# Optimization experiments

Measured on AMD Instinct MI355X. Metric: run time of the kernel, lower is better.

Reference implementation:

```python
import jax, jax.numpy as jnp
import numpy as np

WS = 3
HEADS = 6
C = 192
QK_UNITS = 32
QKC = HEADS * QK_UNITS      # 192
V_UNITS = C // HEADS        # 32
DIL = 1
EPS = 1.55e-05


def _static_kernel():
    # one-hot im2col kernel: output tap i picks window offset (i//WS, i%WS)
    sk = np.zeros((WS, WS, 1, WS * WS), np.float32)
    for i in range(WS * WS):
        sk[i // WS, i % WS, 0, i] = 1.0
    return jnp.asarray(sk)


def _depthwise(x, kernel, dil):
    # TF depthwise_conv2d: kernel [ws,ws,Cin,mult] -> out channel c*mult+m
    ws, _, cin, mult = kernel.shape
    k = kernel.reshape(ws, ws, 1, cin * mult)
    return jax.lax.conv_general_dilated(
        x, k, window_strides=(1, 1), padding='SAME',
        rhs_dilation=(dil, dil),
        dimension_numbers=('NHWC', 'HWIO', 'NHWC'),
        feature_group_count=cin)


def _rel_bias(cpb_w1, cpb_b1, cpb_w2):
    # RelativeBias(query_window=1, key_window=WS, pretrain_window=WS)
    halo = (WS - 1) // 2
    rel = np.arange(-halo, halo + 1, dtype=np.float32)
    rel = np.stack(np.meshgrid(rel, rel, indexing='ij'), axis=-1)  # [WS,WS,2]
    rel = rel * (8.0 / (WS - 1.0))
    rel = np.sign(rel) * np.log1p(np.abs(rel)) / np.log(8.0)
    tab = jnp.asarray(rel.reshape(-1, 2))                 # [WS^2, 2]
    hid = jax.nn.relu(tab @ cpb_w1 + cpb_b1)              # CPB MLP
    bias = jax.nn.sigmoid(hid @ cpb_w2) * 16.0            # [WS^2, HEADS]
    # for query_window==1 the rel_idx gather is a row reversal of the table
    bias = bias[::-1]
    return bias.T                                         # [HEADS, WS^2]


def reference(x, qkv_w, q_bias, v_bias, deformable_kernel, scale,
              cpb_w1, cpb_b1, cpb_w2, proj_w, proj_b):
    B, H, W, _ = x.shape
    sk = _static_kernel()

    # 1x1 qkv conv + (q, 0, v) bias
    qkv = jnp.einsum('bhwc,cd->bhwd', x, qkv_w)
    qkv = qkv + jnp.concatenate([q_bias, jnp.zeros_like(q_bias), v_bias])
    q, k, v = jnp.split(qkv, [QKC, 2 * QKC], axis=-1)

    # deformable + static window extraction (depthwise, multiplier = WS^2)
    k = _depthwise(k, deformable_kernel + sk, DIL)        # [B,H,W,QKC*WS^2]
    v_kernel = deformable_kernel
    if C != QKC:
        v_kernel = jnp.repeat(v_kernel, C // QKC, axis=2)
    v = _depthwise(v, sk + v_kernel, DIL)                 # [B,H,W,C*WS^2]

    q = q.reshape(B, H, W, HEADS, 1, QK_UNITS)
    k = k.reshape(B, H, W, HEADS, QK_UNITS, WS * WS)
    v = v.reshape(B, H, W, HEADS, V_UNITS, WS * WS)

    # tf.math.l2_normalize semantics: x * rsqrt(max(sum(x^2), eps))
    q = q * jax.lax.rsqrt(jnp.maximum(jnp.sum(q * q, -1, keepdims=True), EPS))
    k = k * jax.lax.rsqrt(jnp.maximum(jnp.sum(k * k, -2, keepdims=True), EPS))

    attn = jnp.matmul(q * jnp.exp(scale), k)              # [B,H,W,HEADS,1,WS^2]

    # border mask: zero-padded taps get -100
    ones = jnp.ones((1, H, W, 1), x.dtype)
    valid = _depthwise(ones, sk, DIL).reshape(1, H, W, 1, 1, WS * WS)
    mask = -100.0 * (valid == 0.0).astype(x.dtype)
    rb = _rel_bias(cpb_w1, cpb_b1, cpb_w2).reshape(1, 1, 1, HEADS, 1, WS * WS)
    attn = jax.nn.softmax(attn + mask + rb, axis=-1)

    out = jnp.matmul(attn, jnp.swapaxes(v, -1, -2))       # [B,H,W,HEADS,1,V_UNITS]
    out = out.reshape(B, H, W, C)
    return jnp.einsum('bhwc,cd->bhwd', out, proj_w) + proj_b


def setup_inputs() -> dict:
    key = jax.random.key(0)
    ks = jax.random.split(key, 6)
    return {
        'x': jax.random.normal(ks[0], (4, 96, 96, C), jnp.float32),
        'qkv_w': jax.random.normal(ks[1], (C, 2 * QKC + C), jnp.float32) * (C ** -0.5),
        'q_bias': jnp.zeros((QKC,), jnp.float32),
        'v_bias': jnp.zeros((C,), jnp.float32),
        'deformable_kernel': jax.random.normal(ks[2], (WS, WS, QKC, WS * WS), jnp.float32) * 0.05,
        'scale': jnp.full((HEADS, 1, 1), np.log(10.0), jnp.float32),
        'cpb_w1': jax.random.normal(ks[3], (2, 512), jnp.float32) * 0.5,
        'cpb_b1': jnp.zeros((512,), jnp.float32),
        'cpb_w2': jax.random.normal(ks[4], (512, HEADS), jnp.float32) * (512 ** -0.5),
        'proj_w': jax.random.normal(ks[5], (C, C), jnp.float32) * (C ** -0.5),
        'proj_b': jnp.zeros((C,), jnp.float32),
    }
```

## Files before the change

kernel.cpp:

```cpp
#include <hip/hip_runtime.h>
#include <math.h>

#define EPS 1.55e-05f
#define PIX 36864
#define IMG 9216

typedef __attribute__((ext_vector_type(8))) short short8v;
typedef __attribute__((ext_vector_type(4))) float float4v;
typedef __attribute__((ext_vector_type(4))) unsigned short ushort4v;
typedef __attribute__((ext_vector_type(4))) unsigned int uint4v;

static __device__ __forceinline__ unsigned short f2bf(float f) {
    unsigned u = __float_as_uint(f);
    unsigned r = (u + 0x7FFFu + ((u >> 16) & 1u)) >> 16;
    return (unsigned short)r;
}
static __device__ __forceinline__ float bflo(unsigned d) {
    return __uint_as_float(d << 16);
}
static __device__ __forceinline__ float bfhi(unsigned d) {
    return __uint_as_float(d & 0xffff0000u);
}

__global__ __launch_bounds__(512)
void relbias_kernel(const float* __restrict__ w1, const float* __restrict__ b1,
                    const float* __restrict__ w2, float* __restrict__ rb)
{
    __shared__ float hid[9][512];
    int i = threadIdx.x;
    const float s0 = -0.7739760316291208f, s2 = 0.7739760316291208f;
    float sv[3]; sv[0] = s0; sv[1] = 0.f; sv[2] = s2;
    float w1a = w1[i], w1b = w1[512 + i], bb = b1[i];
    #pragma unroll
    for (int j = 0; j < 9; j++) {
        float t0 = sv[j / 3], t1 = sv[j % 3];
        hid[j][i] = fmaxf(t0 * w1a + t1 * w1b + bb, 0.f);
    }
    __syncthreads();
    if (i < 54) {
        int he = i / 9, t = i % 9, j = 8 - t;
        float acc = 0.f;
        for (int u = 0; u < 512; u++) acc += hid[j][u] * w2[u * 6 + he];
        rb[he * 9 + t] = 16.f / (1.f + expf(-acc));
    }
}

__global__ __launch_bounds__(256)
void prep_kernel(const float* __restrict__ x, const float* __restrict__ qkv_w,
                 const float* __restrict__ proj_w,
                 unsigned short* __restrict__ xs, unsigned short* __restrict__ Bt,
                 unsigned short* __restrict__ Bt2)
{
    int tid = blockIdx.x * 256 + threadIdx.x;
    int stride = gridDim.x * 256;
    int total_x4 = PIX * 192 / 4;
    for (int i = tid; i < total_x4; i += stride) {
        float4 v = ((const float4*)x)[i];
        ushort4v o;
        o.x = f2bf(v.x); o.y = f2bf(v.y); o.z = f2bf(v.z); o.w = f2bf(v.w);
        ((ushort4v*)xs)[i] = o;
    }
    for (int i = tid; i < 576 * 192; i += stride) {
        int n = i / 192, k = i - n * 192;
        Bt[i] = f2bf(qkv_w[k * 576 + n]);
    }
    for (int i = tid; i < 192 * 192; i += stride) {
        int n = i / 192, k = i - n * 192;
        Bt2[i] = f2bf(proj_w[k * 192 + n]);
    }
}

template<int MODE>
__global__ __launch_bounds__(256)
void mfma_gemm_kernel(const unsigned short* __restrict__ Abf,
                      const unsigned short* __restrict__ Btb,
                      void* __restrict__ Cout,
                      const float* __restrict__ bias0,
                      const float* __restrict__ bias1)
{
    const int K = 192;
    __shared__ short smem[128 * 64 + 64 * 64];
    short* As = smem;
    short* Bs = smem + 128 * 64;
    int tid = threadIdx.x;
    int m0 = blockIdx.y * 128;
    int n0 = blockIdx.x * 64;
    int lane = tid & 63, wid = tid >> 6;
    int wm = wid >> 1, wn = wid & 1;
    int lr = lane & 15, lk = lane >> 4;

    float4v acc[4][2];
    #pragma unroll
    for (int a = 0; a < 4; a++)
        #pragma unroll
        for (int b = 0; b < 2; b++)
            #pragma unroll
            for (int e = 0; e < 4; e++) acc[a][b][e] = 0.f;

    int sr = tid >> 3;
    int sc = tid & 7;
    for (int k0 = 0; k0 < K; k0 += 64) {
        #pragma unroll
        for (int i = 0; i < 4; i++) {
            int r = sr + i * 32;
            short8v v = *(const short8v*)(Abf + (size_t)(m0 + r) * K + k0 + sc * 8);
            *(short8v*)(As + r * 64 + ((sc ^ (r & 7)) * 8)) = v;
        }
        #pragma unroll
        for (int i = 0; i < 2; i++) {
            int r = sr + i * 32;
            short8v v = *(const short8v*)(Btb + (size_t)(n0 + r) * K + k0 + sc * 8);
            *(short8v*)(Bs + r * 64 + ((sc ^ (r & 7)) * 8)) = v;
        }
        __syncthreads();
        #pragma unroll
        for (int ks = 0; ks < 2; ks++) {
            short8v af[4], bf[2];
            #pragma unroll
            for (int fm = 0; fm < 4; fm++) {
                int r = wm * 64 + fm * 16 + lr;
                int c = (ks * 4 + lk) ^ (r & 7);
                af[fm] = *(const short8v*)(As + r * 64 + c * 8);
            }
            #pragma unroll
            for (int fn = 0; fn < 2; fn++) {
                int r = wn * 32 + fn * 16 + lr;
                int c = (ks * 4 + lk) ^ (r & 7);
                bf[fn] = *(const short8v*)(Bs + r * 64 + c * 8);
            }
            #pragma unroll
            for (int fm = 0; fm < 4; fm++)
                #pragma unroll
                for (int fn = 0; fn < 2; fn++)
                    acc[fm][fn] = __builtin_amdgcn_mfma_f32_16x16x32_bf16(
                        af[fm], bf[fn], acc[fm][fn], 0, 0, 0);
        }
        __syncthreads();
    }

    if (MODE == 0) {
        const int TP = 74;
        unsigned short* T = (unsigned short*)smem;
        #pragma unroll
        for (int fm = 0; fm < 4; fm++) {
            #pragma unroll
            for (int fn = 0; fn < 2; fn++) {
                int n = wn * 32 + fn * 16 + lr;
                int gn = n0 + n;
                float bv = (gn < 192) ? bias0[gn] : ((gn < 384) ? 0.f : bias1[gn - 384]);
                #pragma unroll
                for (int e = 0; e < 4; e++) {
                    int m = wm * 64 + fm * 16 + lk * 4 + e;
                    T[m * TP + n] = f2bf(acc[fm][fn][e] + bv);
                }
            }
        }
        __syncthreads();
        unsigned short* qkv8 = (unsigned short*)Cout;
        #pragma unroll
        for (int i = 0; i < 4; i++) {
            int u = tid + 256 * i;
            int m = u & 127, cgl = u >> 7;
            short8v vv = *(const short8v*)(T + m * TP + cgl * 8);
            int gcg = (n0 >> 3) + cgl;
            *(short8v*)(qkv8 + ((size_t)gcg * PIX + m0 + m) * 8) = vv;
        }
    } else {
        float* outp = (float*)Cout;
        #pragma unroll
        for (int fm = 0; fm < 4; fm++) {
            #pragma unroll
            for (int fn = 0; fn < 2; fn++) {
                int n = n0 + wn * 32 + fn * 16 + lr;
                float bv = bias0[n];
                #pragma unroll
                for (int e = 0; e < 4; e++) {
                    int m = m0 + wm * 64 + fm * 16 + lk * 4 + e;
                    outp[(size_t)m * 192 + n] = acc[fm][fn][e] + bv;
                }
            }
        }
    }
}

__global__ __launch_bounds__(256)
void fused5_kernel(const unsigned short* __restrict__ qkv8, const float* __restrict__ deform,
                   const float* __restrict__ scale, const float* __restrict__ rb,
                   unsigned short* __restrict__ attnS)
{
    __shared__ float red[64][21];

    int id = blockIdx.x;
    int strip = id % 3;
    int yp = (id / 3) % 48;
    int he = (id / 144) % 6;
    int b = id / 864;
    int tid = threadIdx.x;
    int l = tid & 63;
    int wsub = tid >> 6;
    int X = strip * 32 + (l & 31);
    int Y = yp * 2 + (l >> 5);
    int pimg = Y * 96 + X;
    size_t ibase = (size_t)b * IMG;

    for (int i = tid; i < 64 * 21; i += 256) (&red[0][0])[i] = 0.f;
    __syncthreads();

    int c0 = __builtin_amdgcn_readfirstlane(he * 32 + wsub * 8);
    int qg = c0 >> 3;
    const uint4v* qp = (const uint4v*)(qkv8 + ((size_t)qg * PIX + ibase) * 8);
    const uint4v* kp = (const uint4v*)(qkv8 + ((size_t)(24 + qg) * PIX + ibase) * 8);
    const uint4v* vp = (const uint4v*)(qkv8 + ((size_t)(48 + qg) * PIX + ibase) * 8);

    int off[9];
    unsigned okm = 0;
    #pragma unroll
    for (int pos = 0; pos < 9; pos++) {
        int dy = pos / 3 - 1, dx = pos % 3 - 1;
        int yy = Y + dy, xx = X + dx;
        bool ok = (yy >= 0) && (yy < 96) && (xx >= 0) && (xx < 96);
        okm |= (ok ? 1u : 0u) << pos;
        off[pos] = ok ? (yy * 96 + xx) : pimg;
    }

    uint4v qd = qp[pimg];
    uint4v kd[9];
    #pragma unroll
    for (int pos = 0; pos < 9; pos++) kd[pos] = kp[off[pos]];
    #pragma unroll
    for (int pos = 0; pos < 9; pos++)
        if (!((okm >> pos) & 1)) { kd[pos].x = 0; kd[pos].y = 0; kd[pos].z = 0; kd[pos].w = 0; }

    float qk[9], kn[9];
    #pragma unroll
    for (int t = 0; t < 9; t++) { qk[t] = 0.f; kn[t] = 0.f; }
    float qn2 = 0.f;

    #pragma unroll
    for (int ci = 0; ci < 8; ci++) {
        int c = c0 + ci;
        unsigned qw = ((const unsigned*)&qd)[ci >> 1];
        float q = (ci & 1) ? bfhi(qw) : bflo(qw);
        qn2 = fmaf(q, q, qn2);
        float kin[9];
        #pragma unroll
        for (int pos = 0; pos < 9; pos++) {
            unsigned dw = ((const unsigned*)&kd[pos])[ci >> 1];
            kin[pos] = (ci & 1) ? bfhi(dw) : bflo(dw);
        }
        float ktap[9];
        #pragma unroll
        for (int t = 0; t < 9; t++) ktap[t] = kin[t];
        #pragma unroll
        for (int pos = 0; pos < 9; pos++) {
            const float* wr = deform + ((size_t)pos * 192 + c) * 9;
            #pragma unroll
            for (int t = 0; t < 9; t++) ktap[t] = fmaf(kin[pos], wr[t], ktap[t]);
        }
        #pragma unroll
        for (int t = 0; t < 9; t++) {
            qk[t] = fmaf(q, ktap[t], qk[t]);
            kn[t] = fmaf(ktap[t], ktap[t], kn[t]);
        }
    }

    uint4v vd[9];
    #pragma unroll
    for (int pos = 0; pos < 9; pos++) vd[pos] = vp[off[pos]];

    #pragma unroll
    for (int t = 0; t < 9; t++) atomicAdd(&red[l][t], qk[t]);
    #pragma unroll
    for (int t = 0; t < 9; t++) atomicAdd(&red[l][9 + t], kn[t]);
    atomicAdd(&red[l][18], qn2);

    #pragma unroll
    for (int pos = 0; pos < 9; pos++)
        if (!((okm >> pos) & 1)) { vd[pos].x = 0; vd[pos].y = 0; vd[pos].z = 0; vd[pos].w = 0; }
    __syncthreads();

    float qn = rsqrtf(fmaxf(red[l][18], EPS));
    float es = expf(scale[he]);
    float w[9];
    float m = -1e30f;
    #pragma unroll
    for (int t = 0; t < 9; t++) {
        float lg = es * qn * red[l][t] * rsqrtf(fmaxf(red[l][9 + t], EPS));
        lg += (((okm >> t) & 1) ? 0.f : -100.f) + rb[he * 9 + t];
        w[t] = lg;
        m = fmaxf(m, lg);
    }
    float ssum = 0.f;
    #pragma unroll
    for (int t = 0; t < 9; t++) { w[t] = expf(w[t] - m); ssum += w[t]; }
    float inv = 1.f / ssum;
    #pragma unroll
    for (int t = 0; t < 9; t++) w[t] *= inv;

    unsigned short o8[8];
    #pragma unroll
    for (int ci = 0; ci < 8; ci++) {
        int c = c0 + ci;
        float vin[9];
        #pragma unroll
        for (int pos = 0; pos < 9; pos++) {
            unsigned dw = ((const unsigned*)&vd[pos])[ci >> 1];
            vin[pos] = (ci & 1) ? bfhi(dw) : bflo(dw);
        }
        float acc = 0.f;
        #pragma unroll
        for (int pos = 0; pos < 9; pos++) {
            const float* wr = deform + ((size_t)pos * 192 + c) * 9;
            float sp = w[pos];
            #pragma unroll
            for (int t = 0; t < 9; t++) sp = fmaf(w[t], wr[t], sp);
            acc = fmaf(vin[pos], sp, acc);
        }
        o8[ci] = f2bf(acc);
    }
    short8v ov;
    #pragma unroll
    for (int ci = 0; ci < 8; ci++) ov[ci] = (short)o8[ci];
    *(short8v*)(attnS + (ibase + pimg) * 192 + c0) = ov;
}

extern "C" void kernel_launch(void* const* d_in, const int* in_sizes, int n_in,
                              void* d_out, int out_size, void* d_ws, size_t ws_size,
                              hipStream_t stream) {
    const float* x       = (const float*)d_in[0];
    const float* qkv_w   = (const float*)d_in[1];
    const float* q_bias  = (const float*)d_in[2];
    const float* v_bias  = (const float*)d_in[3];
    const float* deform  = (const float*)d_in[4];
    const float* scale   = (const float*)d_in[5];
    const float* cpb_w1  = (const float*)d_in[6];
    const float* cpb_b1  = (const float*)d_in[7];
    const float* cpb_w2  = (const float*)d_in[8];
    const float* proj_w  = (const float*)d_in[9];
    const float* proj_b  = (const float*)d_in[10];
    float* out = (float*)d_out;

    char* ws = (char*)d_ws;
    float*          rb    = (float*)ws;
    unsigned short* xs    = (unsigned short*)(ws + 256);
    unsigned short* Bt    = (unsigned short*)(ws + 256 + 14155776);
    unsigned short* Bt2   = (unsigned short*)(ws + 256 + 14155776 + 221184);
    unsigned short* qkv8  = (unsigned short*)(ws + 256 + 14155776 + 221184 + 73728);
    unsigned short* attnS = (unsigned short*)(ws + 256 + 14155776 + 221184 + 73728 + 42467328);

    relbias_kernel<<<1, 512, 0, stream>>>(cpb_w1, cpb_b1, cpb_w2, rb);
    prep_kernel<<<2048, 256, 0, stream>>>(x, qkv_w, proj_w, xs, Bt, Bt2);
    mfma_gemm_kernel<0><<<dim3(576 / 64, PIX / 128), 256, 0, stream>>>(
        xs, Bt, (void*)qkv8, q_bias, v_bias);
    fused5_kernel<<<3456, 256, 0, stream>>>(qkv8, deform, scale, rb, attnS);
    mfma_gemm_kernel<1><<<dim3(192 / 64, PIX / 128), 256, 0, stream>>>(
        attnS, Bt2, (void*)out, proj_b, nullptr);
}
```

Before: 291.9 us.

## Stage K/V halo tiles in LDS and use 2D pixel tiles per head

Replaces the fused window-attention kernel with a version that assigns each block a 16x4 pixel tile for one head. The block cooperatively loads the K and V halo (18x6 pixels times 32 channels) into shared memory, and neighbour taps are read from LDS instead of nine redundant global gathers per pixel. Each warp now handles 16 channels instead of 8, and blocks shrink to 128 threads. The aim is to cut redundant global and L2 traffic for overlapping 3x3 windows, at the cost of extra syncs, LDS use and more per-thread work.

After: 270.0 us. 7.5% less time.

```diff
diff --git a/kernel.cpp b/kernel.cpp
--- a/kernel.cpp
+++ b/kernel.cpp
@@ -15,12 +15,8 @@
     unsigned r = (u + 0x7FFFu + ((u >> 16) & 1u)) >> 16;
     return (unsigned short)r;
 }
-static __device__ __forceinline__ float bflo(unsigned d) {
-    return __uint_as_float(d << 16);
-}
-static __device__ __forceinline__ float bfhi(unsigned d) {
-    return __uint_as_float(d & 0xffff0000u);
-}
+static __device__ __forceinline__ float bflo(unsigned d) { return __uint_as_float(d << 16); }
+static __device__ __forceinline__ float bfhi(unsigned d) { return __uint_as_float(d & 0xffff0000u); }
 
 __global__ __launch_bounds__(512)
 void relbias_kernel(const float* __restrict__ w1, const float* __restrict__ b1,
@@ -183,53 +179,74 @@
     }
 }
 
-__global__ __launch_bounds__(256)
-void fused5_kernel(const unsigned short* __restrict__ qkv8, const float* __restrict__ deform,
+__global__ __launch_bounds__(128)
+void fused7_kernel(const unsigned short* __restrict__ qkv8, const float* __restrict__ deform,
                    const float* __restrict__ scale, const float* __restrict__ rb,
                    unsigned short* __restrict__ attnS)
 {
+    __shared__ unsigned short kv[4][108][8];
     __shared__ float red[64][21];
 
     int id = blockIdx.x;
-    int strip = id % 3;
-    int yp = (id / 3) % 48;
-    int he = (id / 144) % 6;
-    int b = id / 864;
+    int he = id % 6;
+    int tile = id / 6;
+    int b = tile / 144;
+    int t2 = tile - b * 144;
+    int x0 = (t2 % 6) * 16, y0 = (t2 / 6) * 4;
     int tid = threadIdx.x;
     int l = tid & 63;
-    int wsub = tid >> 6;
-    int X = strip * 32 + (l & 31);
-    int Y = yp * 2 + (l >> 5);
+    int w = __builtin_amdgcn_readfirstlane(tid >> 6);
+    int lx = l & 15, ly = l >> 4;
+    int X = x0 + lx, Y = y0 + ly;
     int pimg = Y * 96 + X;
     size_t ibase = (size_t)b * IMG;
 
-    for (int i = tid; i < 64 * 21; i += 256) (&red[0][0])[i] = 0.f;
+    for (int i = tid; i < 64 * 21; i += 128) (&red[0][0])[i] = 0.f;
+
+    int g8q = he * 4 + w * 2;
+    uint4v qd[2];
+    qd[0] = *(const uint4v*)(qkv8 + ((size_t)g8q * PIX + ibase + pimg) * 8);
+    qd[1] = *(const uint4v*)(qkv8 + ((size_t)(g8q + 1) * PIX + ibase + pimg) * 8);
+
+    int kgbase = 24 + he * 4;
+    int vgbase = 48 + he * 4;
+    #pragma unroll
+    for (int r = 0; r < 4; r++) {
+        int i = tid + r * 128;
+        if (i < 432) {
+            int gg = i / 108, hp = i - gg * 108;
+            int hy = hp / 18, hx = hp - hy * 18;
+            int gx = x0 - 1 + hx, gy = y0 - 1 + hy;
+            bool ok = (gx >= 0) && (gx < 96) && (gy >= 0) && (gy < 96);
+            uint4v v; v.x = 0; v.y = 0; v.z = 0; v.w = 0;
+            if (ok) v = *(const uint4v*)(qkv8 + ((size_t)(kgbase + gg) * PIX + ibase + gy * 96 + gx) * 8);
+            *(uint4v*)&kv[gg][hp][0] = v;
+        }
+    }
+    uint4v vst[4];
+    #pragma unroll
+    for (int r = 0; r < 4; r++) {
+        int i = tid + r * 128;
+        vst[r].x = 0; vst[r].y = 0; vst[r].z = 0; vst[r].w = 0;
+        if (i < 432) {
+            int gg = i / 108, hp = i - gg * 108;
+            int hy = hp / 18, hx = hp - hy * 18;
+            int gx = x0 - 1 + hx, gy = y0 - 1 + hy;
+            bool ok = (gx >= 0) && (gx < 96) && (gy >= 0) && (gy < 96);
+            if (ok) vst[r] = *(const uint4v*)(qkv8 + ((size_t)(vgbase + gg) * PIX + ibase + gy * 96 + gx) * 8);
+        }
+    }
     __syncthreads();
 
-    int c0 = __builtin_amdgcn_readfirstlane(he * 32 + wsub * 8);
-    int qg = c0 >> 3;
-    const uint4v* qp = (const uint4v*)(qkv8 + ((size_t)qg * PIX + ibase) * 8);
-    const uint4v* kp = (const uint4v*)(qkv8 + ((size_t)(24 + qg) * PIX + ibase) * 8);
-    const uint4v* vp = (const uint4v*)(qkv8 + ((size_t)(48 + qg) * PIX + ibase) * 8);
-
-    int off[9];
     unsigned okm = 0;
     #pragma unroll
     for (int pos = 0; pos < 9; pos++) {
         int dy = pos / 3 - 1, dx = pos % 3 - 1;
-        int yy = Y + dy, xx = X + dx;
-        bool ok = (yy >= 0) && (yy < 96) && (xx >= 0) && (xx < 96);
+        bool ok = (Y + dy >= 0) && (Y + dy < 96) && (X + dx >= 0) && (X + dx < 96);
         okm |= (ok ? 1u : 0u) << pos;
-        off[pos] = ok ? (yy * 96 + xx) : pimg;
-    }
-
-    uint4v qd = qp[pimg];
-    uint4v kd[9];
-    #pragma unroll
-    for (int pos = 0; pos < 9; pos++) kd[pos] = kp[off[pos]];
-    #pragma unroll
-    for (int pos = 0; pos < 9; pos++)
-        if (!((okm >> pos) & 1)) { kd[pos].x = 0; kd[pos].y = 0; kd[pos].z = 0; kd[pos].w = 0; }
+    }
+    const int hp0 = (ly + 1) * 18 + (lx + 1);
+    const int dtap[9] = {-19, -18, -17, -1, 0, 1, 17, 18, 19};
 
     float qk[9], kn[9];
     #pragma unroll
@@ -237,91 +254,111 @@
     float qn2 = 0.f;
 
     #pragma unroll
-    for (int ci = 0; ci < 8; ci++) {
-        int c = c0 + ci;
-        unsigned qw = ((const unsigned*)&qd)[ci >> 1];
-        float q = (ci & 1) ? bfhi(qw) : bflo(qw);
-        qn2 = fmaf(q, q, qn2);
-        float kin[9];
-        #pragma unroll
-        for (int pos = 0; pos < 9; pos++) {
-            unsigned dw = ((const unsigned*)&kd[pos])[ci >> 1];
-            kin[pos] = (ci & 1) ? bfhi(dw) : bflo(dw);
-        }
-        float ktap[9];
-        #pragma unroll
-        for (int t = 0; t < 9; t++) ktap[t] = kin[t];
-        #pragma unroll
-        for (int pos = 0; pos < 9; pos++) {
-            const float* wr = deform + ((size_t)pos * 192 + c) * 9;
-            #pragma unroll
-            for (int t = 0; t < 9; t++) ktap[t] = fmaf(kin[pos], wr[t], ktap[t]);
-        }
-        #pragma unroll
-        for (int t = 0; t < 9; t++) {
-            qk[t] = fmaf(q, ktap[t], qk[t]);
-            kn[t] = fmaf(ktap[t], ktap[t], kn[t]);
-        }
-    }
-
-    uint4v vd[9];
-    #pragma unroll
-    for (int pos = 0; pos < 9; pos++) vd[pos] = vp[off[pos]];
+    for (int g = 0; g < 2; g++) {
+        int g8 = w * 2 + g;
+        uint4v kd[9];
+        #pragma unroll
+        for (int pos = 0; pos < 9; pos++)
+            kd[pos] = *(const uint4v*)&kv[g8][hp0 + dtap[pos]][0];
+        #pragma unroll
+        for (int ci = 0; ci < 8; ci++) {
+            int c = he * 32 + (w * 2 + g) * 8 + ci;
+            unsigned qw = ((const unsigned*)&qd[g])[ci >> 1];
+            float q = (ci & 1) ? bfhi(qw) : bflo(qw);
+            qn2 = fmaf(q, q, qn2);
+            float kin[9];
+            #pragma unroll
+            for (int pos = 0; pos < 9; pos++) {
+                unsigned dw = ((const unsigned*)&kd[pos])[ci >> 1];
+                kin[pos] = (ci & 1) ? bfhi(dw) : bflo(dw);
+            }
+            float ktap[9];
+            #pragma unroll
+            for (int t = 0; t < 9; t++) ktap[t] = kin[t];
+            #pragma unroll
+            for (int pos = 0; pos < 9; pos++) {
+                const float* wr = deform + ((size_t)pos * 192 + c) * 9;
+                #pragma unroll
+                for (int t = 0; t < 9; t++) ktap[t] = fmaf(kin[pos], wr[t], ktap[t]);
+            }
+            #pragma unroll
+            for (int t = 0; t < 9; t++) {
+                qk[t] = fmaf(q, ktap[t], qk[t]);
+                kn[t] = fmaf(ktap[t], ktap[t], kn[t]);
+            }
+        }
+    }
 
     #pragma unroll
     for (int t = 0; t < 9; t++) atomicAdd(&red[l][t], qk[t]);
     #pragma unroll
     for (int t = 0; t < 9; t++) atomicAdd(&red[l][9 + t], kn[t]);
     atomicAdd(&red[l][18], qn2);
-
-    #pragma unroll
-    for (int pos = 0; pos < 9; pos++)
-        if (!((okm >> pos) & 1)) { vd[pos].x = 0; vd[pos].y = 0; vd[pos].z = 0; vd[pos].w = 0; }
     __syncthreads();
 
     float qn = rsqrtf(fmaxf(red[l][18], EPS));
     float es = expf(scale[he]);
-    float w[9];
+    float wgt[9];
     float m = -1e30f;
     #pragma unroll
     for (int t = 0; t < 9; t++) {
         float lg = es * qn * red[l][t] * rsqrtf(fmaxf(red[l][9 + t], EPS));
         lg += (((okm >> t) & 1) ? 0.f : -100.f) + rb[he * 9 + t];
-        w[t] = lg;
+        wgt[t] = lg;
         m = fmaxf(m, lg);
     }
     float ssum = 0.f;
     #pragma unroll
-    for (int t = 0; t < 9; t++) { w[t] = expf(w[t] - m); ssum += w[t]; }
+    for (int t = 0; t < 9; t++) { wgt[t] = expf(wgt[t] - m); ssum += wgt[t]; }
     float inv = 1.f / ssum;
     #pragma unroll
-    for (int t = 0; t < 9; t++) w[t] *= inv;
-
-    unsigned short o8[8];
-    #pragma unroll
-    for (int ci = 0; ci < 8; ci++) {
-        int c = c0 + ci;
-        float vin[9];
-        #pragma unroll
-        for (int pos = 0; pos < 9; pos++) {
-            unsigned dw = ((const unsigned*)&vd[pos])[ci >> 1];
-            vin[pos] = (ci & 1) ? bfhi(dw) : bflo(dw);
-        }
-        float acc = 0.f;
-        #pragma unroll
-        for (int pos = 0; pos < 9; pos++) {
-            const float* wr = deform + ((size_t)pos * 192 + c) * 9;
-            float sp = w[pos];
-            #pragma unroll
-            for (int t = 0; t < 9; t++) sp = fmaf(w[t], wr[t], sp);
-            acc = fmaf(vin[pos], sp, acc);
-        }
-        o8[ci] = f2bf(acc);
-    }
-    short8v ov;
-    #pragma unroll
-    for (int ci = 0; ci < 8; ci++) ov[ci] = (short)o8[ci];
-    *(short8v*)(attnS + (ibase + pimg) * 192 + c0) = ov;
+    for (int t = 0; t < 9; t++) wgt[t] *= inv;
+
+    #pragma unroll
+    for (int r = 0; r < 4; r++) {
+        int i = tid + r * 128;
+        if (i < 432) {
+            int gg = i / 108, hp = i - gg * 108;
+            *(uint4v*)&kv[gg][hp][0] = vst[r];
+        }
+    }
+    __syncthreads();
+
+    unsigned short o16[16];
+    #pragma unroll
+    for (int g = 0; g < 2; g++) {
+        int g8 = w * 2 + g;
+        uint4v vd[9];
+        #pragma unroll
+        for (int pos = 0; pos < 9; pos++)
+            vd[pos] = *(const uint4v*)&kv[g8][hp0 + dtap[pos]][0];
+        #pragma unroll
+        for (int ci = 0; ci < 8; ci++) {
+            int c = he * 32 + (w * 2 + g) * 8 + ci;
+            float vin[9];
+            #pragma unroll
+            for (int pos = 0; pos < 9; pos++) {
+                unsigned dw = ((const unsigned*)&vd[pos])[ci >> 1];
+                vin[pos] = (ci & 1) ? bfhi(dw) : bflo(dw);
+            }
+            float acc = 0.f;
+            #pragma unroll
+            for (int pos = 0; pos < 9; pos++) {
+                const float* wr = deform + ((size_t)pos * 192 + c) * 9;
+                float sp = wgt[pos];
+                #pragma unroll
+                for (int t = 0; t < 9; t++) sp = fmaf(wgt[t], wr[t], sp);
+                acc = fmaf(vin[pos], sp, acc);
+            }
+            o16[g * 8 + ci] = f2bf(acc);
+        }
+    }
+    unsigned short* orow = attnS + (ibase + pimg) * 192 + he * 32 + w * 16;
+    short8v ov0, ov1;
+    #pragma unroll
+    for (int ci = 0; ci < 8; ci++) { ov0[ci] = (short)o16[ci]; ov1[ci] = (short)o16[8 + ci]; }
+    *(short8v*)(orow) = ov0;
+    *(short8v*)(orow + 8) = ov1;
 }
 
 extern "C" void kernel_launch(void* const* d_in, const int* in_sizes, int n_in,
@@ -352,7 +389,7 @@
     prep_kernel<<<2048, 256, 0, stream>>>(x, qkv_w, proj_w, xs, Bt, Bt2);
     mfma_gemm_kernel<0><<<dim3(576 / 64, PIX / 128), 256, 0, stream>>>(
         xs, Bt, (void*)qkv8, q_bias, v_bias);
-    fused5_kernel<<<3456, 256, 0, stream>>>(qkv8, deform, scale, rb, attnS);
+    fused7_kernel<<<3456, 128, 0, stream>>>(qkv8, deform, scale, rb, attnS);
     mfma_gemm_kernel<1><<<dim3(192 / 64, PIX / 128), 256, 0, stream>>>(
         attnS, Bt2, (void*)out, proj_b, nullptr);
 }
```
